# Kernel tuning notes

Hardware: AMD Instinct MI355X
Metric: run time of the kernel (lower is better)

Reference implementation:

```python
import jax, jax.numpy as jnp
import numpy as np

N = 4  # hypercomplex dimension

def setup_inputs() -> dict:
    key = jax.random.key(0)
    k1, k2, k3 = jax.random.split(key, 3)
    x = jax.random.normal(k1, (32, 196, 768), dtype=jnp.float32)
    # [n, out_pad/n, in_pad/n] = [4, 3072//4, 768//4]
    weight_components = jax.random.normal(k2, (N, 768, 192), dtype=jnp.float32) * 0.02
    bias = jax.random.normal(k3, (3072,), dtype=jnp.float32) * 0.02
    return {"x": x, "weight_components": weight_components, "bias": bias}

def reference(x, weight_components, bias):
    n, out_blk, in_blk = weight_components.shape
    batch_shape = x.shape[:-1]
    xb = x.reshape(-1, n, in_blk)  # [B, n, in_blk]
    # original: out[:, (i+j)%n] += x[:, j] @ W[i].T
    # equivalently out[:, k] = sum_j x[:, j] @ W[(k-j)%n].T
    k_idx = jnp.arange(n)[:, None]
    j_idx = jnp.arange(n)[None, :]
    Wperm = weight_components[(k_idx - j_idx) % n]  # [n(k), n(j), out_blk, in_blk]
    out = jnp.einsum('bjc,kjoc->bko', xb, Wperm)    # [B, n, out_blk]
    out = out.reshape(-1, n * out_blk) + bias
    return out.reshape(*batch_shape, n * out_blk)
```

## Files before the change

### kernel.cpp

```cpp
#include <hip/hip_runtime.h>
#include <stdint.h>

#define M_ROWS 6272
#define K_DIM  768
#define N_DIM  3072
#define BM 128
#define BN 256
#define BK 32
#define NITER (K_DIM / BK)

#define X_CHUNKS (M_ROWS * K_DIM / 8)
#define W_CHUNKS (N_DIM * K_DIM / 8)
#define X_BLOCKS (X_CHUNKS / 256)
#define W_BLOCKS (W_CHUNKS / 256)

#define GRID_X (N_DIM / BN)
#define GRID_Y (M_ROWS / BM)
#define NWG    (GRID_X * GRID_Y)

typedef unsigned short u16;
typedef __attribute__((ext_vector_type(8))) __bf16 bf16x8;
typedef __attribute__((ext_vector_type(4))) float f32x4;

__device__ __forceinline__ u16 f32_to_bf16(float f) {
    unsigned u = __float_as_uint(f);
    unsigned r = 0x7FFFu + ((u >> 16) & 1u);
    return (u16)((u + r) >> 16);
}

__device__ __forceinline__ unsigned pack2(float a, float b) {
    return (unsigned)f32_to_bf16(a) | ((unsigned)f32_to_bf16(b) << 16);
}

#define GLOAD16(gp, lp) __builtin_amdgcn_global_load_lds( \
    (const __attribute__((address_space(1))) void*)(gp),  \
    (__attribute__((address_space(3))) void*)(lp), 16, 0, 0)

__global__ void prep_kernel(const float* __restrict__ x, const float* __restrict__ w,
                            u16* __restrict__ xb, u16* __restrict__ wb) {
    int b = blockIdx.x;
    if (b < X_BLOCKS) {
        int idx = b * 256 + threadIdx.x;
        const float4* xp = (const float4*)x + (size_t)idx * 2;
        float4 a = xp[0], c = xp[1];
        uint4 v;
        v.x = pack2(a.x, a.y);
        v.y = pack2(a.z, a.w);
        v.z = pack2(c.x, c.y);
        v.w = pack2(c.z, c.w);
        ((uint4*)xb)[idx] = v;
    } else {
        int idx = (b - X_BLOCKS) * 256 + threadIdx.x;
        int n    = idx / 96;
        int kc   = idx - n * 96;
        int kblk = n / 768;
        int o    = n - kblk * 768;
        int j    = kc / 24;
        int c8   = kc - j * 24;
        int i    = (kblk - j) & 3;
        const float* src = w + (((size_t)i * 768 + o) * 192 + c8 * 8);
        float4 a = ((const float4*)src)[0];
        float4 c = ((const float4*)src)[1];
        uint4 v;
        v.x = pack2(a.x, a.y);
        v.y = pack2(a.z, a.w);
        v.z = pack2(c.x, c.y);
        v.w = pack2(c.z, c.w);
        ((uint4*)wb)[idx] = v;
    }
}

__global__ __launch_bounds__(256, 2) void gemm_bt(
    const u16* __restrict__ A,
    const u16* __restrict__ B,
    const float* __restrict__ bias,
    float* __restrict__ C)
{
    __shared__ __align__(16) u16 As[2][BM * BK];
    __shared__ __align__(16) u16 Bs[2][BN * BK];

    const int orig = blockIdx.x;
    const int xcd  = orig & 7;
    const int pos  = orig >> 3;
    const int q    = NWG >> 3;
    const int r    = NWG & 7;
    const int lin  = (xcd < r ? xcd * (q + 1) : r * (q + 1) + (xcd - r) * q) + pos;
    const int rowBlk = lin / GRID_X;
    const int colBlk = lin - rowBlk * GRID_X;

    const int rowBase = rowBlk * BM;
    const int colBase = colBlk * BN;

    const int tid    = threadIdx.x;
    const int wave   = tid >> 6;
    const int lane   = tid & 63;
    const int lane16 = lane & 15;
    const int quad   = lane >> 4;
    const int wc     = wave;

    const int rA = tid >> 2;
    const int sA = (tid & 3) ^ ((rA >> 1) & 3);

    const uint4* Ag = (const uint4*)(A + (size_t)(rowBase + rA) * K_DIM + sA * 8);
    const uint4* Bg = (const uint4*)(B + (size_t)(colBase + rA) * K_DIM + sA * 8);
    const int rowStride = 64 * (K_DIM / 8);

    char* AsB = (char*)As + wave * 1024;
    char* BsB = (char*)Bs + wave * 1024;

#define ISSUE(g, b) do {                                                    \
        GLOAD16(Ag + (g) * 4,                 AsB + (b) * 8192);            \
        GLOAD16(Ag + (g) * 4 + rowStride,     AsB + (b) * 8192 + 4096);     \
        GLOAD16(Bg + (g) * 4,                 BsB + (b) * 16384);           \
        GLOAD16(Bg + (g) * 4 + rowStride,     BsB + (b) * 16384 + 4096);    \
        GLOAD16(Bg + (g) * 4 + 2 * rowStride, BsB + (b) * 16384 + 8192);    \
        GLOAD16(Bg + (g) * 4 + 3 * rowStride, BsB + (b) * 16384 + 12288);   \
    } while (0)

    const int swz  = (lane16 >> 1) & 3;
    const int slot = (quad ^ swz) * 8;
    int aoff[8], boff[4];
#pragma unroll
    for (int i = 0; i < 8; ++i)
        aoff[i] = (i * 16 + lane16) * BK + slot;
#pragma unroll
    for (int j = 0; j < 4; ++j)
        boff[j] = (wc * 64 + j * 16 + lane16) * BK + slot;

    f32x4 acc[8][4] = {};

#define DS_READS(cb)                                                        \
    _Pragma("unroll") for (int i = 0; i < 8; ++i)                           \
        af[i] = *(const bf16x8*)&As[cb][aoff[i]];                           \
    _Pragma("unroll") for (int j = 0; j < 4; ++j)                           \
        bfv[j] = *(const bf16x8*)&Bs[cb][boff[j]];

#define MFMA32()                                                            \
    __builtin_amdgcn_s_setprio(1);                                          \
    _Pragma("unroll") for (int i = 0; i < 8; ++i)                           \
    _Pragma("unroll") for (int j = 0; j < 4; ++j)                           \
        acc[i][j] = __builtin_amdgcn_mfma_f32_16x16x32_bf16(                \
            af[i], bfv[j], acc[i][j], 0, 0, 0);                             \
    __builtin_amdgcn_s_setprio(0);

#define ITER(cur, nxt, g) {                                                 \
        bf16x8 af[8], bfv[4];                                               \
        ISSUE(g, nxt);                                                      \
        asm volatile("s_waitcnt vmcnt(6)" ::: "memory");                    \
        asm volatile("s_barrier" ::: "memory");                             \
        DS_READS(cur)                                                       \
        asm volatile("s_waitcnt lgkmcnt(0)" ::: "memory");                  \
        asm volatile("s_barrier" ::: "memory");                             \
        MFMA32()                                                            \
    }

#define ITER_LAST(cur) {                                                    \
        bf16x8 af[8], bfv[4];                                               \
        asm volatile("s_waitcnt vmcnt(0)" ::: "memory");                    \
        asm volatile("s_barrier" ::: "memory");                             \
        DS_READS(cur)                                                       \
        MFMA32()                                                            \
    }

    ISSUE(0, 0);

    for (int t = 0; t < 22; t += 2) {
        ITER(0, 1, t + 1);
        ITER(1, 0, t + 2);
    }
    ITER(0, 1, 23);
    ITER_LAST(1);

    float bv[4];
#pragma unroll
    for (int j = 0; j < 4; ++j)
        bv[j] = bias[colBase + wc * 64 + j * 16 + lane16];
#pragma unroll
    for (int i = 0; i < 8; ++i) {
        int row0 = rowBase + i * 16 + quad * 4;
#pragma unroll
        for (int r2 = 0; r2 < 4; ++r2) {
            float* cp = C + (size_t)(row0 + r2) * N_DIM + colBase + wc * 64 + lane16;
#pragma unroll
            for (int j = 0; j < 4; ++j)
                cp[j * 16] = acc[i][j][r2] + bv[j];
        }
    }
#undef ISSUE
#undef DS_READS
#undef MFMA32
#undef ITER
#undef ITER_LAST
}

extern "C" void kernel_launch(void* const* d_in, const int* in_sizes, int n_in,
                              void* d_out, int out_size, void* d_ws, size_t ws_size,
                              hipStream_t stream) {
    const float* x    = (const float*)d_in[0];
    const float* w    = (const float*)d_in[1];
    const float* bias = (const float*)d_in[2];
    float* out = (float*)d_out;

    u16* xb = (u16*)d_ws;
    u16* wb = (u16*)((char*)d_ws + (size_t)M_ROWS * K_DIM * 2);

    hipLaunchKernelGGL(prep_kernel, dim3(X_BLOCKS + W_BLOCKS), dim3(256),
                       0, stream, x, w, xb, wb);
    hipLaunchKernelGGL(gemm_bt, dim3(NWG), dim3(256),
                       0, stream, xb, wb, bias, out);
}
```

Measured before the change: 143.8 us.

## Deepen GEMM LDS pipeline to six stages with two-subtile epochs

The shared-memory ring grows from 2 to 6 K-tile buffers. Each epoch now processes two K-subtiles and issues global-to-LDS loads four tiles ahead, with a single wait and barrier per epoch instead of two barriers per tile. The goal is to hide global load latency and cut synchronisation overhead. The trade-off is about 144 KB of LDS per workgroup, which likely allows only one workgroup per CU instead of the two the launch bounds target.

```diff
diff --git a/kernel.cpp b/kernel.cpp
--- a/kernel.cpp
+++ b/kernel.cpp
@@ -76,8 +76,8 @@
     const float* __restrict__ bias,
     float* __restrict__ C)
 {
-    __shared__ __align__(16) u16 As[2][BM * BK];
-    __shared__ __align__(16) u16 Bs[2][BN * BK];
+    __shared__ __align__(16) u16 As[6][BM * BK];
+    __shared__ __align__(16) u16 Bs[6][BN * BK];
 
     const int orig = blockIdx.x;
     const int xcd  = orig & 7;
@@ -143,33 +143,46 @@
             af[i], bfv[j], acc[i][j], 0, 0, 0);                             \
     __builtin_amdgcn_s_setprio(0);
 
-#define ITER(cur, nxt, g) {                                                 \
+#define SUBTILE(cb) {                                                       \
         bf16x8 af[8], bfv[4];                                               \
-        ISSUE(g, nxt);                                                      \
-        asm volatile("s_waitcnt vmcnt(6)" ::: "memory");                    \
-        asm volatile("s_barrier" ::: "memory");                             \
-        DS_READS(cur)                                                       \
-        asm volatile("s_waitcnt lgkmcnt(0)" ::: "memory");                  \
-        asm volatile("s_barrier" ::: "memory");                             \
+        DS_READS(cb)                                                        \
         MFMA32()                                                            \
     }
 
-#define ITER_LAST(cur) {                                                    \
-        bf16x8 af[8], bfv[4];                                               \
+#define EPOCH(s0, fb, g) {                                                  \
+        { bf16x8 af[8], bfv[4];                                             \
+          DS_READS(s0)                                                      \
+          ISSUE((g), (fb)); ISSUE((g) + 1, (fb) + 1);                       \
+          MFMA32() }                                                        \
+        SUBTILE((s0) + 1)                                                   \
+        asm volatile("s_waitcnt vmcnt(12)" ::: "memory");                   \
+        asm volatile("s_waitcnt lgkmcnt(0)\n\ts_barrier" ::: "memory");     \
+    }
+
+#define EPOCH_DRAIN(s0) {                                                   \
+        SUBTILE(s0)                                                         \
+        SUBTILE((s0) + 1)                                                   \
         asm volatile("s_waitcnt vmcnt(0)" ::: "memory");                    \
-        asm volatile("s_barrier" ::: "memory");                             \
-        DS_READS(cur)                                                       \
-        MFMA32()                                                            \
-    }
-
-    ISSUE(0, 0);
-
-    for (int t = 0; t < 22; t += 2) {
-        ITER(0, 1, t + 1);
-        ITER(1, 0, t + 2);
-    }
-    ITER(0, 1, 23);
-    ITER_LAST(1);
+        asm volatile("s_waitcnt lgkmcnt(0)\n\ts_barrier" ::: "memory");     \
+    }
+
+#define EPOCH_LAST(s0) {                                                    \
+        SUBTILE(s0)                                                         \
+        SUBTILE((s0) + 1)                                                   \
+    }
+
+    ISSUE(0, 0); ISSUE(1, 1);
+    ISSUE(2, 2); ISSUE(3, 3);
+    asm volatile("s_waitcnt vmcnt(12)\n\ts_barrier" ::: "memory");
+
+    for (int k6 = 0; k6 < 18; k6 += 6) {
+        EPOCH(0, 4, k6 + 4);
+        EPOCH(2, 0, k6 + 6);
+        EPOCH(4, 2, k6 + 8);
+    }
+    EPOCH(0, 4, 22);
+    EPOCH_DRAIN(2);
+    EPOCH_LAST(4);
 
     float bv[4];
 #pragma unroll
@@ -189,8 +202,10 @@
 #undef ISSUE
 #undef DS_READS
 #undef MFMA32
-#undef ITER
-#undef ITER_LAST
+#undef SUBTILE
+#undef EPOCH
+#undef EPOCH_DRAIN
+#undef EPOCH_LAST
 }
 
 extern "C" void kernel_launch(void* const* d_in, const int* in_sizes, int n_in,
```

Measured after the change: 150.3 us. 1.05x slower.
